# Kernel optimization log

Measured on AMD Instinct MI355X. Metric: run time of the kernel, lower is better.

The kernel has to match this reference:

```python
import jax, jax.numpy as jnp
import numpy as np

L, D, H, DFF = 12, 768, 12, 3072
DH = D // H
EPS = 1e-5


def _layer_norm(x, g, b):
    # manual LN as in source: biased variance, eps inside sqrt
    mean = jnp.mean(x, axis=-1, keepdims=True)
    var = jnp.mean((x - mean) ** 2, axis=-1, keepdims=True)
    return g * (x - mean) / jnp.sqrt(var + EPS) + b


def setup_inputs() -> dict:
    key = jax.random.key(0)
    ks = jax.random.split(key, 10)
    x = jax.random.normal(ks[0], (8, 512, D), dtype=jnp.float32)
    mask = jnp.zeros((8, 1, 1, 512), dtype=jnp.float32)
    s = 0.02
    Wq = jax.random.normal(ks[1], (L, D, D), jnp.float32) * s
    Wk = jax.random.normal(ks[2], (L, D, D), jnp.float32) * s
    Wv = jax.random.normal(ks[3], (L, D, D), jnp.float32) * s
    Wo = jax.random.normal(ks[4], (L, D, D), jnp.float32) * s
    W1 = jax.random.normal(ks[5], (L, DFF, D), jnp.float32) * s
    W2 = jax.random.normal(ks[6], (L, D, DFF), jnp.float32) * s
    z = lambda *sh: jnp.zeros(sh, jnp.float32)
    o = lambda *sh: jnp.ones(sh, jnp.float32)
    return {
        'x': x, 'mask': mask,
        'Wq': Wq, 'bq': z(L, D), 'Wk': Wk, 'bk': z(L, D), 'Wv': Wv, 'bv': z(L, D),
        'Wo': Wo, 'bo': z(L, D), 'g1': o(L, D), 'b1': z(L, D),
        'W1': W1, 'bf1': z(L, DFF), 'W2': W2, 'bf2': z(L, D),
        'g2': o(L, D), 'b2': z(L, D),
    }


def reference(x, mask, Wq, bq, Wk, bk, Wv, bv, Wo, bo, g1, b1, W1, bf1, W2, bf2, g2, b2):
    B, S, _ = x.shape
    scale = 1.0 / jnp.sqrt(jnp.float32(DH))

    def layer(h, p):
        wq, pq, wk, pk, wv, pv, wo, po, gg1, bb1, w1, pf1, w2, pf2, gg2, bb2 = p
        # Dense: x @ W^T + b
        q = (h @ wq.T + pq).reshape(B, S, H, DH).transpose(0, 2, 1, 3)  # [B,H,S,dh]
        k = (h @ wk.T + pk).reshape(B, S, H, DH).transpose(0, 2, 1, 3)
        v = (h @ wv.T + pv).reshape(B, S, H, DH).transpose(0, 2, 1, 3)
        scores = jnp.einsum('bhqd,bhkd->bhqk', q, k) * scale
        scores = scores + mask * -1e9
        attn = jax.nn.softmax(scores, axis=-1)
        ctx = jnp.einsum('bhqk,bhkd->bhqd', attn, v)
        ctx = ctx.transpose(0, 2, 1, 3).reshape(B, S, D)
        a = _layer_norm(h + (ctx @ wo.T + po), gg1, bb1)
        ffn = jnp.maximum(a @ w1.T + pf1, 0.0) @ w2.T + pf2
        out = _layer_norm(a + ffn, gg2, bb2)
        return out, None

    params = (Wq, bq, Wk, bk, Wv, bv, Wo, bo, g1, b1, W1, bf1, W2, bf2, g2, b2)
    out, _ = jax.lax.scan(layer, x, params)
    return out
```

## Files before the change

### kernel.cpp

```cpp
#include <hip/hip_runtime.h>
#include <hip/hip_bf16.h>
#include <stdint.h>

#define DDIM 768
#define NH 12
#define DHD 64
#define DFF 3072
#define NLAYER 12
#define SEQ 512
#define NB 8
#define ROWS (NB*SEQ)
#define QS   2304

typedef __attribute__((ext_vector_type(4))) float f32x4;
typedef __attribute__((ext_vector_type(8))) short short8;

#define S_BARRIER()  asm volatile("s_barrier" ::: "memory")
#define WAIT_LGKM0() asm volatile("s_waitcnt lgkmcnt(0)" ::: "memory")
#define WAIT_VM0()   asm volatile("s_waitcnt vmcnt(0)" ::: "memory")
#define WAIT_VM3()   asm volatile("s_waitcnt vmcnt(3)" ::: "memory")
#define WAIT_VM4()   asm volatile("s_waitcnt vmcnt(4)" ::: "memory")

static __device__ __forceinline__ short bf16r(float f) {
  union { float f; uint32_t u; } a; a.f = f;
  uint32_t u = a.u;
  u += 0x7FFFu + ((u >> 16) & 1u);
  return (short)(u >> 16);
}

static __device__ __forceinline__ float bf2f(short s) {
  union { uint32_t u; float f; } c;
  c.u = ((uint32_t)(uint16_t)s) << 16;
  return c.f;
}

static __device__ __forceinline__ f32x4 mfma_bf16(short8 a, short8 b, f32x4 c) {
  return __builtin_amdgcn_mfma_f32_16x16x32_bf16(a, b, c, 0, 0, 0);
}

static __device__ __forceinline__ void gload16(const void* g, void* l) {
  __builtin_amdgcn_global_load_lds(
      (__attribute__((address_space(1))) void*)(void*)(uintptr_t)g,
      (__attribute__((address_space(3))) void*)l,
      16, 0, 0);
}

#define WDD    589824
#define WFD    2359296
#define WLAYER (4*WDD + 2*WFD)

struct WAll {
  const float* src[7];
  short* wb;
  short* xb;
};

__global__ void wconv_all_kernel(WAll wa) {
  const int y = blockIdx.y;
  const float* __restrict__ src = wa.src[y];
  if (y == 6) {
    short* __restrict__ dst = wa.xb;
    const int n8 = (ROWS * DDIM) / 8;
    for (int i = blockIdx.x * 256 + threadIdx.x; i < n8; i += gridDim.x * 256) {
      f32x4 a = *(const f32x4*)(src + (size_t)i * 8);
      f32x4 b = *(const f32x4*)(src + (size_t)i * 8 + 4);
      short8 o;
      o[0] = bf16r(a[0]); o[1] = bf16r(a[1]); o[2] = bf16r(a[2]); o[3] = bf16r(a[3]);
      o[4] = bf16r(b[0]); o[5] = bf16r(b[1]); o[6] = bf16r(b[2]); o[7] = bf16r(b[3]);
      *(short8*)(dst + (size_t)i * 8) = o;
    }
    return;
  }
  const int perL8  = (y < 4 ? WDD : WFD) / 8;
  const int dstOff = (y < 4) ? y * WDD : 4 * WDD + (y - 4) * WFD;
  const int tot    = NLAYER * perL8;
  for (int i = blockIdx.x * 256 + threadIdx.x; i < tot; i += gridDim.x * 256) {
    const int l = i / perL8;
    const int r = i - l * perL8;
    f32x4 a = *(const f32x4*)(src + (size_t)i * 8);
    f32x4 b = *(const f32x4*)(src + (size_t)i * 8 + 4);
    short8 o;
    o[0] = bf16r(a[0]); o[1] = bf16r(a[1]); o[2] = bf16r(a[2]); o[3] = bf16r(a[3]);
    o[4] = bf16r(b[0]); o[5] = bf16r(b[1]); o[6] = bf16r(b[2]); o[7] = bf16r(b[3]);
    *(short8*)(wa.wb + (size_t)l * WLAYER + dstOff + (size_t)r * 8) = o;
  }
}

__global__ void bcat_kernel(const float* __restrict__ bq, const float* __restrict__ bk,
                            const float* __restrict__ bv, float* __restrict__ out) {
  const int idx = blockIdx.x * 256 + threadIdx.x;
  if (idx >= NLAYER * QS) return;
  const int l = idx / QS;
  const int j = idx - l * QS;
  float v;
  if (j < DDIM)            v = bq[l * DDIM + j];
  else if (j < 2 * DDIM)   v = bk[l * DDIM + j - DDIM];
  else                     v = bv[l * DDIM + j - 2 * DDIM];
  out[idx] = v;
}

template<int OUTMODE, int BM>
__launch_bounds__(256, 4)
__global__ void gemm_bt(const short* __restrict__ A, const short* __restrict__ W,
                        const float* __restrict__ bias, void* __restrict__ outp,
                        int M, int N, int K) {
  constexpr int MF  = BM / 32;
  constexpr int ISS = BM / 64;

  __shared__ __align__(16) short As[2][BM * 32];
  __shared__ __align__(16) short Bs[2][128 * 32];

  const int tid  = threadIdx.x;
  const int lane = tid & 63;
  const int wid  = tid >> 6;
  const int l16  = lane & 15;
  const int kg   = lane >> 4;
  const int wr   = wid >> 1;
  const int wc   = wid & 1;
  const int m0   = blockIdx.x * BM;
  const int n0   = blockIdx.y * 128;

  const f32x4 zero = {0.f, 0.f, 0.f, 0.f};
  f32x4 acc[MF][4];
  #pragma unroll
  for (int i = 0; i < MF; i++)
    #pragma unroll
    for (int j = 0; j < 4; j++) acc[i][j] = zero;

  const int lrow = lane >> 2;
  const int lcol = (lane & 3) * 8;
  const short* Ag = A + (size_t)(m0 + wid * (BM / 4) + lrow) * K + lcol;
  const short* Wg = W + (size_t)(n0 + wid * 32 + lrow) * K + lcol;

  auto stage = [&](int buf, int k0) {
    #pragma unroll
    for (int j = 0; j < ISS; j++)
      gload16(Ag + k0 + (size_t)(j * 16) * K, &As[buf][(wid * (BM / 4) + j * 16) * 32]);
    #pragma unroll
    for (int j = 0; j < 2; j++)
      gload16(Wg + k0 + (size_t)(j * 16) * K, &Bs[buf][(wid * 32 + j * 16) * 32]);
  };

  const int nsteps = K >> 5;
  stage(0, 0);
  stage(1, 32);
  if (ISS == 2) { WAIT_VM4(); } else { WAIT_VM3(); }
  S_BARRIER();

  for (int t = 0; t < nsteps; ++t) {
    const int cur = t & 1;
    short8 af[MF], bfr[4];
    #pragma unroll
    for (int i = 0; i < MF; i++)
      af[i] = *(const short8*)&As[cur][(wr * (BM / 2) + i * 16 + l16) * 32 + kg * 8];
    #pragma unroll
    for (int j = 0; j < 4; j++)
      bfr[j] = *(const short8*)&Bs[cur][(wc * 64 + j * 16 + l16) * 32 + kg * 8];
    WAIT_LGKM0();
    S_BARRIER();

    const bool pf = (t + 2 < nsteps);
    if (pf) stage(cur, (t + 2) << 5);
    __builtin_amdgcn_sched_barrier(0);
    #pragma unroll
    for (int i = 0; i < MF; i++)
      #pragma unroll
      for (int j = 0; j < 4; j++)
        acc[i][j] = mfma_bf16(af[i], bfr[j], acc[i][j]);
    __builtin_amdgcn_sched_barrier(0);

    if (pf) { if (ISS == 2) { WAIT_VM4(); } else { WAIT_VM3(); } }
    else    { WAIT_VM0(); }
    S_BARRIER();
  }

  float* outf = (float*)outp;
  short* outb = (short*)outp;
  #pragma unroll
  for (int j = 0; j < 4; j++) {
    const int col = n0 + wc * 64 + j * 16 + l16;
    const float bv = bias[col];
    #pragma unroll
    for (int i = 0; i < MF; i++) {
      const int row0 = m0 + wr * (BM / 2) + i * 16 + kg * 4;
      #pragma unroll
      for (int e = 0; e < 4; e++) {
        float v = acc[i][j][e] + bv;
        if (OUTMODE == 2) v = fmaxf(v, 0.0f);
        const size_t off = (size_t)(row0 + e) * N + col;
        if (OUTMODE == 0) outf[off] = v;
        else              outb[off] = bf16r(v);
      }
    }
  }
}

__launch_bounds__(256, 2)
__global__ void attn_kernel(const short* __restrict__ QKV, const float* __restrict__ mask,
                            short* __restrict__ ctx) {
  __shared__ __align__(16) short Vt[64 * 512];

  const int bh = blockIdx.x;
  const int b = bh / NH;
  const int h = bh % NH;
  const int tid  = threadIdx.x;
  const int lane = tid & 63;
  const int wid  = tid >> 6;
  const int l16  = lane & 15;
  const int kg   = lane >> 4;

  const short* Qb = QKV + (size_t)b * SEQ * QS + h * DHD;
  const short* Kb = Qb + DDIM;
  const short* Vb = Qb + 2 * DDIM;

  for (int c = tid; c < SEQ * 8; c += 256) {
    const int kv = c >> 3;
    const int d0 = (c & 7) * 8;
    short8 v = *(const short8*)(Vb + (size_t)kv * QS + d0);
    #pragma unroll
    for (int j = 0; j < 8; j++)
      Vt[(d0 + j) * 512 + (kv ^ ((j & 3) << 3))] = v[j];
  }
  __syncthreads();

  const int q0 = blockIdx.y * 128 + wid * 32;

  short8 qf[2][2];
  #pragma unroll
  for (int rt = 0; rt < 2; rt++)
    #pragma unroll
    for (int dh = 0; dh < 2; dh++)
      qf[rt][dh] = *(const short8*)(Qb + (size_t)(q0 + rt * 16 + l16) * QS + dh * 32 + kg * 8);

  float mrun[2] = {-1e30f, -1e30f};
  float lrun[2] = {0.0f, 0.0f};
  const f32x4 zero = {0.f, 0.f, 0.f, 0.f};
  f32x4 oacc[2][4];
  #pragma unroll
  for (int rt = 0; rt < 2; rt++)
    #pragma unroll
    for (int dt = 0; dt < 4; dt++) oacc[rt][dt] = zero;

  const float* maskb = mask + (size_t)b * SEQ;

  for (int kv0 = 0; kv0 < SEQ; kv0 += 32) {
    short8 kf[2][2];
    #pragma unroll
    for (int kvh = 0; kvh < 2; kvh++)
      #pragma unroll
      for (int dh = 0; dh < 2; dh++)
        kf[kvh][dh] = *(const short8*)(Kb + (size_t)(kv0 + kvh * 16 + l16) * QS + dh * 32 + kg * 8);

    short8 vf[4];
    #pragma unroll
    for (int dt = 0; dt < 4; dt++) {
      const int d = dt * 16 + l16;
      vf[dt] = *(const short8*)&Vt[d * 512 + ((kv0 + kg * 8) ^ ((d & 3) << 3))];
    }

    const f32x4 mq0 = *(const f32x4*)(maskb + kv0 + kg * 4);
    const f32x4 mq1 = *(const f32x4*)(maskb + kv0 + 16 + kg * 4);

    #pragma unroll
    for (int rt = 0; rt < 2; rt++) {
      f32x4 s0 = zero, s1 = zero;
      s0 = mfma_bf16(kf[0][0], qf[rt][0], s0);
      s0 = mfma_bf16(kf[0][1], qf[rt][1], s0);
      s1 = mfma_bf16(kf[1][0], qf[rt][0], s1);
      s1 = mfma_bf16(kf[1][1], qf[rt][1], s1);

      float p[8];
      #pragma unroll
      for (int e = 0; e < 4; e++) {
        p[e]     = s0[e] * 0.125f + mq0[e] * (-1e9f);
        p[e + 4] = s1[e] * 0.125f + mq1[e] * (-1e9f);
      }
      float mt = p[0];
      #pragma unroll
      for (int e = 1; e < 8; e++) mt = fmaxf(mt, p[e]);
      mt = fmaxf(mt, __shfl_xor(mt, 16, 64));
      mt = fmaxf(mt, __shfl_xor(mt, 32, 64));
      const float mnew = fmaxf(mrun[rt], mt);
      const float corr = __expf(mrun[rt] - mnew);
      float ts = 0.0f;
      #pragma unroll
      for (int e = 0; e < 8; e++) { p[e] = __expf(p[e] - mnew); ts += p[e]; }
      ts += __shfl_xor(ts, 16, 64);
      ts += __shfl_xor(ts, 32, 64);
      lrun[rt] = lrun[rt] * corr + ts;
      mrun[rt] = mnew;

      const int P0 = (int)(((uint32_t)(uint16_t)bf16r(p[1]) << 16) | (uint16_t)bf16r(p[0]));
      const int P1 = (int)(((uint32_t)(uint16_t)bf16r(p[3]) << 16) | (uint16_t)bf16r(p[2]));
      const int P2 = (int)(((uint32_t)(uint16_t)bf16r(p[5]) << 16) | (uint16_t)bf16r(p[4]));
      const int P3 = (int)(((uint32_t)(uint16_t)bf16r(p[7]) << 16) | (uint16_t)bf16r(p[6]));
      const int sl0 = (((2 * kg) & 3) << 4) + l16;
      const int sl1 = (((2 * kg + 1) & 3) << 4) + l16;
      const int x0 = __shfl(P0, sl0, 64), y0 = __shfl(P2, sl0, 64);
      const int x1 = __shfl(P1, sl0, 64), y1 = __shfl(P3, sl0, 64);
      const int x2 = __shfl(P0, sl1, 64), y2 = __shfl(P2, sl1, 64);
      const int x3 = __shfl(P1, sl1, 64), y3 = __shfl(P3, sl1, 64);
      union { int w[4]; short8 v; } pa;
      const bool hi = (kg >= 2);
      pa.w[0] = hi ? y0 : x0;
      pa.w[1] = hi ? y1 : x1;
      pa.w[2] = hi ? y2 : x2;
      pa.w[3] = hi ? y3 : x3;

      const float c0 = __shfl(corr, kg * 4 + 0, 64);
      const float c1 = __shfl(corr, kg * 4 + 1, 64);
      const float c2 = __shfl(corr, kg * 4 + 2, 64);
      const float c3 = __shfl(corr, kg * 4 + 3, 64);

      #pragma unroll
      for (int dt = 0; dt < 4; dt++) {
        f32x4 o = oacc[rt][dt];
        o[0] *= c0; o[1] *= c1; o[2] *= c2; o[3] *= c3;
        oacc[rt][dt] = mfma_bf16(pa.v, vf[dt], o);
      }
    }
  }

  short* cb = ctx + (size_t)b * SEQ * DDIM + h * DHD;
  #pragma unroll
  for (int rt = 0; rt < 2; rt++) {
    const float li = 1.0f / lrun[rt];
    const float l0 = __shfl(li, kg * 4 + 0, 64);
    const float l1 = __shfl(li, kg * 4 + 1, 64);
    const float l2 = __shfl(li, kg * 4 + 2, 64);
    const float l3 = __shfl(li, kg * 4 + 3, 64);
    #pragma unroll
    for (int dt = 0; dt < 4; dt++) {
      const f32x4 o = oacc[rt][dt];
      const int col = dt * 16 + l16;
      const size_t base = (size_t)(q0 + rt * 16 + kg * 4) * DDIM + col;
      cb[base + 0 * DDIM] = bf16r(o[0] * l0);
      cb[base + 1 * DDIM] = bf16r(o[1] * l1);
      cb[base + 2 * DDIM] = bf16r(o[2] * l2);
      cb[base + 3 * DDIM] = bf16r(o[3] * l3);
    }
  }
}

template<int PBF16>
__launch_bounds__(256, 4)
__global__ void ln_kernel(const float* __restrict__ resid, const void* __restrict__ projv,
                          const float* __restrict__ gw, const float* __restrict__ bw,
                          float* __restrict__ outf, short* __restrict__ outb) {
  const int lane = threadIdx.x & 63;
  const int wid  = threadIdx.x >> 6;
  const int row  = blockIdx.x * 4 + wid;
  const float* rp = resid + (size_t)row * DDIM;
  float v[12];
  float s = 0.0f;
  #pragma unroll
  for (int c = 0; c < 12; c++) {
    float pv;
    if (PBF16) pv = bf2f(((const short*)projv)[(size_t)row * DDIM + c * 64 + lane]);
    else       pv = ((const float*)projv)[(size_t)row * DDIM + c * 64 + lane];
    v[c] = rp[c * 64 + lane] + pv;
    s += v[c];
  }
  #pragma unroll
  for (int o = 1; o < 64; o <<= 1) s += __shfl_xor(s, o, 64);
  const float mean = s * (1.0f / 768.0f);
  float q = 0.0f;
  #pragma unroll
  for (int c = 0; c < 12; c++) { const float d = v[c] - mean; q += d * d; }
  #pragma unroll
  for (int o = 1; o < 64; o <<= 1) q += __shfl_xor(q, o, 64);
  const float inv = 1.0f / sqrtf(q * (1.0f / 768.0f) + 1e-5f);
  #pragma unroll
  for (int c = 0; c < 12; c++) {
    const int idx = c * 64 + lane;
    const float y = gw[idx] * (v[c] - mean) * inv + bw[idx];
    outf[(size_t)row * DDIM + idx] = y;
    outb[(size_t)row * DDIM + idx] = bf16r(y);
  }
}

extern "C" void kernel_launch(void* const* d_in, const int* in_sizes, int n_in,
                              void* d_out, int out_size, void* d_ws, size_t ws_size,
                              hipStream_t stream) {
  const float* x    = (const float*)d_in[0];
  const float* mask = (const float*)d_in[1];
  const float* Wq   = (const float*)d_in[2];
  const float* bq   = (const float*)d_in[3];
  const float* Wk   = (const float*)d_in[4];
  const float* bk   = (const float*)d_in[5];
  const float* Wv   = (const float*)d_in[6];
  const float* bv   = (const float*)d_in[7];
  const float* Wo   = (const float*)d_in[8];
  const float* bo   = (const float*)d_in[9];
  const float* g1   = (const float*)d_in[10];
  const float* b1   = (const float*)d_in[11];
  const float* W1   = (const float*)d_in[12];
  const float* bf1  = (const float*)d_in[13];
  const float* W2   = (const float*)d_in[14];
  const float* bf2  = (const float*)d_in[15];
  const float* g2   = (const float*)d_in[16];
  const float* b2   = (const float*)d_in[17];

  const size_t SD = (size_t)ROWS * DDIM;

  char* ws = (char*)d_ws;
  float* H0   = (float*)ws;  ws += SD * 4;
  short* Bbuf = (short*)ws;  ws += SD * 2;
  short* QKVb = (short*)ws;  ws += (size_t)ROWS * QS * 2;
  short* Cb   = (short*)ws;  ws += SD * 2;
  float* Pf   = (float*)ws;  ws += SD * 4;
  short* F1   = (short*)ws;  ws += (size_t)ROWS * DFF * 2;
  float* Bqkv = (float*)ws;  ws += (size_t)NLAYER * QS * 4;
  short* WB   = (short*)ws;

  {
    WAll wa{};
    wa.src[0] = Wq; wa.src[1] = Wk; wa.src[2] = Wv; wa.src[3] = Wo;
    wa.src[4] = W1; wa.src[5] = W2; wa.src[6] = x;
    wa.wb = WB; wa.xb = Bbuf;
    wconv_all_kernel<<<dim3(1024, 7), 256, 0, stream>>>(wa);
    bcat_kernel<<<dim3((NLAYER * QS + 255) / 256), 256, 0, stream>>>(bq, bk, bv, Bqkv);
  }

  for (int l = 0; l < NLAYER; l++) {
    const short* WL = WB + (size_t)l * WLAYER;

    gemm_bt<1, 128><<<dim3(32, 18), 256, 0, stream>>>(
        Bbuf, WL, Bqkv + (size_t)l * QS, QKVb, ROWS, QS, DDIM);

    attn_kernel<<<dim3(NB * NH, 4), 256, 0, stream>>>(QKVb, mask, Cb);

    gemm_bt<0, 64><<<dim3(64, 6), 256, 0, stream>>>(
        Cb, WL + 3 * WDD, bo + (size_t)l * DDIM, Pf, ROWS, DDIM, DDIM);

    ln_kernel<0><<<dim3(ROWS / 4), 256, 0, stream>>>(l ? H0 : x, Pf,
                                                     g1 + (size_t)l * DDIM, b1 + (size_t)l * DDIM,
                                                     H0, Bbuf);

    gemm_bt<2, 128><<<dim3(32, 24), 256, 0, stream>>>(
        Bbuf, WL + 4 * WDD, bf1 + (size_t)l * DFF, F1, ROWS, DFF, DDIM);

    gemm_bt<1, 64><<<dim3(64, 6), 256, 0, stream>>>(
        F1, WL + 4 * WDD + WFD, bf2 + (size_t)l * DDIM, Bbuf, ROWS, DDIM, DFF);

    ln_kernel<1><<<dim3(ROWS / 4), 256, 0, stream>>>(H0, Bbuf,
                                                     g2 + (size_t)l * DDIM, b2 + (size_t)l * DDIM,
                                                     (l == NLAYER - 1) ? (float*)d_out : H0,
                                                     Bbuf);
  }
}
```

Measured before the change: 2.238 ms.

## Split weight/x conversion kernels, bf16 Wo output, setprio in attention, relax launch bounds

Splits the fused weight and input conversion kernel into a per-layer 3D grid with no loop, plus a separate input conversion kernel. Writes the output projection result in bf16 instead of fp32 and feeds it to the bf16 LayerNorm path, halving that intermediate's traffic at some precision cost. Raises wave priority around the MFMA blocks in attention and lowers the GEMM launch-bounds occupancy hint from 4 to 3 to allow more registers. It also uses a separate buffer for the FFN output so it no longer aliases the LN input buffer.

Measured after the change: 2.222 ms. No clear change (-0.7%).

```diff
diff --git a/kernel.cpp b/kernel.cpp
--- a/kernel.cpp
+++ b/kernel.cpp
@@ -50,40 +50,36 @@
 #define WLAYER (4*WDD + 2*WFD)
 
 struct WAll {
-  const float* src[7];
+  const float* src[6];
   short* wb;
-  short* xb;
 };
 
 __global__ void wconv_all_kernel(WAll wa) {
   const int y = blockIdx.y;
-  const float* __restrict__ src = wa.src[y];
-  if (y == 6) {
-    short* __restrict__ dst = wa.xb;
-    const int n8 = (ROWS * DDIM) / 8;
-    for (int i = blockIdx.x * 256 + threadIdx.x; i < n8; i += gridDim.x * 256) {
-      f32x4 a = *(const f32x4*)(src + (size_t)i * 8);
-      f32x4 b = *(const f32x4*)(src + (size_t)i * 8 + 4);
-      short8 o;
-      o[0] = bf16r(a[0]); o[1] = bf16r(a[1]); o[2] = bf16r(a[2]); o[3] = bf16r(a[3]);
-      o[4] = bf16r(b[0]); o[5] = bf16r(b[1]); o[6] = bf16r(b[2]); o[7] = bf16r(b[3]);
-      *(short8*)(dst + (size_t)i * 8) = o;
-    }
-    return;
-  }
-  const int perL8  = (y < 4 ? WDD : WFD) / 8;
-  const int dstOff = (y < 4) ? y * WDD : 4 * WDD + (y - 4) * WFD;
-  const int tot    = NLAYER * perL8;
-  for (int i = blockIdx.x * 256 + threadIdx.x; i < tot; i += gridDim.x * 256) {
-    const int l = i / perL8;
-    const int r = i - l * perL8;
-    f32x4 a = *(const f32x4*)(src + (size_t)i * 8);
-    f32x4 b = *(const f32x4*)(src + (size_t)i * 8 + 4);
-    short8 o;
-    o[0] = bf16r(a[0]); o[1] = bf16r(a[1]); o[2] = bf16r(a[2]); o[3] = bf16r(a[3]);
-    o[4] = bf16r(b[0]); o[5] = bf16r(b[1]); o[6] = bf16r(b[2]); o[7] = bf16r(b[3]);
-    *(short8*)(wa.wb + (size_t)l * WLAYER + dstOff + (size_t)r * 8) = o;
-  }
+  const int l = blockIdx.z;
+  const int n8 = (y < 4) ? (WDD / 8) : (WFD / 8);
+  const int i = blockIdx.x * 256 + threadIdx.x;
+  if (i >= n8) return;
+  const size_t perL   = (y < 4) ? WDD : WFD;
+  const int    dstOff = (y < 4) ? y * WDD : 4 * WDD + (y - 4) * WFD;
+  const float* __restrict__ src = wa.src[y] + (size_t)l * perL + (size_t)i * 8;
+  short* __restrict__ dst = wa.wb + (size_t)l * WLAYER + dstOff + (size_t)i * 8;
+  f32x4 a = *(const f32x4*)(src);
+  f32x4 b = *(const f32x4*)(src + 4);
+  short8 o;
+  o[0] = bf16r(a[0]); o[1] = bf16r(a[1]); o[2] = bf16r(a[2]); o[3] = bf16r(a[3]);
+  o[4] = bf16r(b[0]); o[5] = bf16r(b[1]); o[6] = bf16r(b[2]); o[7] = bf16r(b[3]);
+  *(short8*)dst = o;
+}
+
+__global__ void xconv_kernel(const float* __restrict__ src, short* __restrict__ dst) {
+  const int i = blockIdx.x * 256 + threadIdx.x;
+  f32x4 a = *(const f32x4*)(src + (size_t)i * 8);
+  f32x4 b = *(const f32x4*)(src + (size_t)i * 8 + 4);
+  short8 o;
+  o[0] = bf16r(a[0]); o[1] = bf16r(a[1]); o[2] = bf16r(a[2]); o[3] = bf16r(a[3]);
+  o[4] = bf16r(b[0]); o[5] = bf16r(b[1]); o[6] = bf16r(b[2]); o[7] = bf16r(b[3]);
+  *(short8*)(dst + (size_t)i * 8) = o;
 }
 
 __global__ void bcat_kernel(const float* __restrict__ bq, const float* __restrict__ bk,
@@ -100,7 +96,7 @@
 }
 
 template<int OUTMODE, int BM>
-__launch_bounds__(256, 4)
+__launch_bounds__(256, 3)
 __global__ void gemm_bt(const short* __restrict__ A, const short* __restrict__ W,
                         const float* __restrict__ bias, void* __restrict__ outp,
                         int M, int N, int K) {
@@ -264,10 +260,12 @@
     #pragma unroll
     for (int rt = 0; rt < 2; rt++) {
       f32x4 s0 = zero, s1 = zero;
+      __builtin_amdgcn_s_setprio(1);
       s0 = mfma_bf16(kf[0][0], qf[rt][0], s0);
       s0 = mfma_bf16(kf[0][1], qf[rt][1], s0);
       s1 = mfma_bf16(kf[1][0], qf[rt][0], s1);
       s1 = mfma_bf16(kf[1][1], qf[rt][1], s1);
+      __builtin_amdgcn_s_setprio(0);
 
       float p[8];
       #pragma unroll
@@ -312,12 +310,14 @@
       const float c2 = __shfl(corr, kg * 4 + 2, 64);
       const float c3 = __shfl(corr, kg * 4 + 3, 64);
 
+      __builtin_amdgcn_s_setprio(1);
       #pragma unroll
       for (int dt = 0; dt < 4; dt++) {
         f32x4 o = oacc[rt][dt];
         o[0] *= c0; o[1] *= c1; o[2] *= c2; o[3] *= c3;
         oacc[rt][dt] = mfma_bf16(pa.v, vf[dt], o);
       }
+      __builtin_amdgcn_s_setprio(0);
     }
   }
 
@@ -408,7 +408,7 @@
   short* Bbuf = (short*)ws;  ws += SD * 2;
   short* QKVb = (short*)ws;  ws += (size_t)ROWS * QS * 2;
   short* Cb   = (short*)ws;  ws += SD * 2;
-  float* Pf   = (float*)ws;  ws += SD * 4;
+  short* Pb   = (short*)ws;  ws += SD * 2;
   short* F1   = (short*)ws;  ws += (size_t)ROWS * DFF * 2;
   float* Bqkv = (float*)ws;  ws += (size_t)NLAYER * QS * 4;
   short* WB   = (short*)ws;
@@ -416,9 +416,10 @@
   {
     WAll wa{};
     wa.src[0] = Wq; wa.src[1] = Wk; wa.src[2] = Wv; wa.src[3] = Wo;
-    wa.src[4] = W1; wa.src[5] = W2; wa.src[6] = x;
-    wa.wb = WB; wa.xb = Bbuf;
-    wconv_all_kernel<<<dim3(1024, 7), 256, 0, stream>>>(wa);
+    wa.src[4] = W1; wa.src[5] = W2;
+    wa.wb = WB;
+    wconv_all_kernel<<<dim3(1152, 6, NLAYER), 256, 0, stream>>>(wa);
+    xconv_kernel<<<dim3((int)(SD / 8 / 256)), 256, 0, stream>>>(x, Bbuf);
     bcat_kernel<<<dim3((NLAYER * QS + 255) / 256), 256, 0, stream>>>(bq, bk, bv, Bqkv);
   }
 
@@ -430,10 +431,10 @@
 
     attn_kernel<<<dim3(NB * NH, 4), 256, 0, stream>>>(QKVb, mask, Cb);
 
-    gemm_bt<0, 64><<<dim3(64, 6), 256, 0, stream>>>(
-        Cb, WL + 3 * WDD, bo + (size_t)l * DDIM, Pf, ROWS, DDIM, DDIM);
-
-    ln_kernel<0><<<dim3(ROWS / 4), 256, 0, stream>>>(l ? H0 : x, Pf,
+    gemm_bt<1, 64><<<dim3(64, 6), 256, 0, stream>>>(
+        Cb, WL + 3 * WDD, bo + (size_t)l * DDIM, Pb, ROWS, DDIM, DDIM);
+
+    ln_kernel<1><<<dim3(ROWS / 4), 256, 0, stream>>>(l ? H0 : x, Pb,
                                                      g1 + (size_t)l * DDIM, b1 + (size_t)l * DDIM,
                                                      H0, Bbuf);
 
@@ -441,9 +442,9 @@
         Bbuf, WL + 4 * WDD, bf1 + (size_t)l * DFF, F1, ROWS, DFF, DDIM);
 
     gemm_bt<1, 64><<<dim3(64, 6), 256, 0, stream>>>(
-        F1, WL + 4 * WDD + WFD, bf2 + (size_t)l * DDIM, Bbuf, ROWS, DDIM, DFF);
-
-    ln_kernel<1><<<dim3(ROWS / 4), 256, 0, stream>>>(H0, Bbuf,
+        F1, WL + 4 * WDD + WFD, bf2 + (size_t)l * DDIM, Pb, ROWS, DDIM, DFF);
+
+    ln_kernel<1><<<dim3(ROWS / 4), 256, 0, stream>>>(H0, Pb,
                                                      g2 + (size_t)l * DDIM, b2 + (size_t)l * DDIM,
                                                      (l == NLAYER - 1) ? (float*)d_out : H0,
                                                      Bbuf);
```
